# Performance work log

Hardware: AMD Instinct MI355X
Metric: run time of the kernel (lower is better)

Reference implementation:

```python
import jax, jax.numpy as jnp
import numpy as np

TOPK = 20
BN_EPS = 1e-5
NEG_SLOPE = 0.2  # DGL GAT default leaky_relu slope


def setup_inputs() -> dict:
    B, N, Ft, D = 128, 512, 64, 64
    key = jax.random.key(0)
    ks = jax.random.split(key, 6)
    return {
        "data": jax.random.normal(ks[0], (B, N, Ft), jnp.float32),
        "emb": jax.random.normal(ks[1], (N, D), jnp.float32) * 0.5,
        "fc_w": jax.random.normal(ks[2], (D, Ft), jnp.float32) * (1.0 / np.sqrt(Ft)),
        "fc_b": jnp.zeros((D,), jnp.float32),
        "attn_w": jax.random.normal(ks[3], (4 * D,), jnp.float32) * (1.0 / np.sqrt(4 * D)),
        "attn_b": jnp.zeros((), jnp.float32),
        "bn_gamma": jnp.ones((D,), jnp.float32),
        "bn_beta": jnp.zeros((D,), jnp.float32),
        "out_w": jax.random.normal(ks[4], (D,), jnp.float32) * (1.0 / np.sqrt(D)),
        "out_b": jnp.zeros((), jnp.float32),
    }


def reference(data, emb, fc_w, fc_b, attn_w, attn_b, bn_gamma, bn_beta, out_w, out_b):
    B, N, Ft = data.shape
    D = emb.shape[-1]

    # --- dynamic graph build from detached embeddings (cosine-sim topk) ---
    w = jax.lax.stop_gradient(emb)
    nrm = jnp.linalg.norm(w, axis=-1)
    cos = (w @ w.T) / (nrm[:, None] * nrm[None, :])      # [N, N]
    _, topk_idx = jax.lax.top_k(cos, TOPK)               # [N, TOPK]
    src = topk_idx.reshape(-1)                           # gated_j (message sources)
    dst = jnp.tile(jnp.arange(N), TOPK)                  # gated_i = arange(N).repeat(1,topk).flatten()

    # --- GAT layer: z = W x + b ; edge score from concat([z, emb]) at both ends ---
    z = jnp.einsum("bnf,df->bnd", data, fc_w) + fc_b     # [B, N, D]
    key_feat = jnp.concatenate([z, jnp.broadcast_to(emb, (B, N, D))], axis=-1)  # [B, N, 2D]
    a_src, a_dst = attn_w[: 2 * D], attn_w[2 * D :]
    s_src = jnp.einsum("bnd,d->bn", key_feat, a_src)
    s_dst = jnp.einsum("bnd,d->bn", key_feat, a_dst)
    e = jax.nn.leaky_relu(s_src[:, src] + s_dst[:, dst] + attn_b, NEG_SLOPE)    # [B, E]

    # segment softmax over incoming edges of each dst node (same edges every batch)
    m = jnp.full((B, N), -jnp.inf, e.dtype).at[:, dst].max(e)
    p = jnp.exp(e - m[:, dst])
    denom = jnp.zeros((B, N), e.dtype).at[:, dst].add(p)
    alpha = p / denom[:, dst]                            # [B, E]

    # scatter-aggregate messages
    h = jnp.zeros_like(z).at[:, dst].add(alpha[..., None] * z[:, src])          # [B, N, D]

    # --- trailing dense: mul by embedding, BatchNorm1d over channel D, relu, linear ---
    rst = h * emb[None]                                  # [B, N, D]
    mu = rst.mean(axis=(0, 1))
    var = rst.var(axis=(0, 1))
    rst = jax.nn.relu((rst - mu) / jnp.sqrt(var + BN_EPS) * bn_gamma + bn_beta)
    out = jnp.einsum("bnd,d->bn", rst, out_w) + out_b    # [B, N]
    return out
```

## Files before the change

### kernel.cpp

```cpp
#include <hip/hip_runtime.h>
#include <hip/hip_bf16.h>

#define NN 512
#define DD 64
#define TOPK 20
#define BB 128

__global__ __launch_bounds__(256) void kdot_pre(const float* __restrict__ emb,
                                                const float* __restrict__ attn_w,
                                                double* __restrict__ cosM,
                                                double* __restrict__ nrm,
                                                float* __restrict__ es_src,
                                                float* __restrict__ es_dst,
                                                double* __restrict__ gstats) {
    __shared__ __align__(16) char smem[17408];
    const int bid = blockIdx.x, t = threadIdx.x;

    if (bid < 256) {
        const int bi0 = (bid >> 4) * 32;
        const int bj0 = (bid & 15) * 32;
        float4* A4 = (float4*)smem;
        float4* B4 = (float4*)(smem + 8704);
        const float4* e4 = (const float4*)emb;

        for (int m = t; m < 512; m += 256) {
            const int r = m >> 4, c = m & 15;
            A4[r * 17 + c] = e4[(bi0 + r) * 16 + c];
            B4[r * 17 + c] = e4[(bj0 + r) * 16 + c];
        }
        __syncthreads();

        const int tr = t >> 4, tc = t & 15;
        #pragma unroll
        for (int rr = 0; rr < 2; ++rr) {
            #pragma unroll
            for (int cc = 0; cc < 2; ++cc) {
                const int r  = tr + rr * 16;
                const int cl = tc + cc * 16;
                double dot = 0.0;
                #pragma unroll
                for (int c = 0; c < 16; ++c) {
                    const float4 a = A4[r * 17 + c];
                    const float4 b = B4[cl * 17 + c];
                    dot += (double)a.x * (double)b.x;
                    dot += (double)a.y * (double)b.y;
                    dot += (double)a.z * (double)b.z;
                    dot += (double)a.w * (double)b.w;
                }
                cosM[(long)(bi0 + r) * NN + (bj0 + cl)] = dot;
            }
        }
    } else if (bid < 258) {
        const int j = (bid - 256) * 256 + t;
        const float4* e4 = (const float4*)emb;
        double s = 0.0;
        #pragma unroll
        for (int c = 0; c < 16; ++c) {
            const float4 v = e4[j * 16 + c];
            const double vx = v.x, vy = v.y, vz = v.z, vw = v.w;
            s += vx * vx; s += vy * vy; s += vz * vz; s += vw * vw;
        }
        nrm[j] = sqrt(s);
        if (bid == 256 && t < 128) gstats[t] = 0.0;
    } else {
        const int j = (bid - 258) * 256 + t;
        float s1 = 0.f, s2 = 0.f;
        #pragma unroll
        for (int c = 0; c < 64; ++c) {
            const float w = emb[j * 64 + c];
            s1 += w * attn_w[64 + c];
            s2 += w * attn_w[192 + c];
        }
        es_src[j] = s1;
        es_dst[j] = s2;
    }
}

__global__ __launch_bounds__(256) void kgemm_sel(const float* __restrict__ data,
                                                 const float* __restrict__ fc_w,
                                                 const float* __restrict__ fc_b,
                                                 const float* __restrict__ attn_w,
                                                 const double* __restrict__ cosM,
                                                 const double* __restrict__ nrmArr,
                                                 float* __restrict__ z,
                                                 float* __restrict__ zsrc,
                                                 float* __restrict__ zdst,
                                                 int* __restrict__ topk) {
    __shared__ __align__(16) char smem[34816];
    const int bid = blockIdx.x, t = threadIdx.x;

    if (bid < 1024) {
        float (*As)[68]  = (float(*)[68])smem;
        float (*WsT)[68] = (float(*)[68])(smem + 17408);
        const long r0 = (long)bid * 64;
        const float4* data4 = (const float4*)data;
        const float4* fcw4  = (const float4*)fc_w;

        for (int m = t; m < 1024; m += 256) {
            const int r = m >> 4, c4 = m & 15;
            *(float4*)&As[r][c4 * 4] = data4[(r0 + r) * 16 + c4];
        }
        for (int m = t; m < 1024; m += 256) {
            const int d = m >> 4, f4 = m & 15;
            float4 v = fcw4[d * 16 + f4];
            WsT[f4 * 4 + 0][d] = v.x;
            WsT[f4 * 4 + 1][d] = v.y;
            WsT[f4 * 4 + 2][d] = v.z;
            WsT[f4 * 4 + 3][d] = v.w;
        }
        __syncthreads();

        const int tr = t >> 4, tc = t & 15;
        float acc[4][4] = {};
        for (int k0 = 0; k0 < 64; k0 += 4) {
            float4 a4[4], b4[4];
            #pragma unroll
            for (int i = 0; i < 4; ++i) a4[i] = *(float4*)&As[tr * 4 + i][k0];
            #pragma unroll
            for (int kk = 0; kk < 4; ++kk) b4[kk] = *(float4*)&WsT[k0 + kk][tc * 4];
            #pragma unroll
            for (int i = 0; i < 4; ++i) {
                acc[i][0] += a4[i].x * b4[0].x + a4[i].y * b4[1].x + a4[i].z * b4[2].x + a4[i].w * b4[3].x;
                acc[i][1] += a4[i].x * b4[0].y + a4[i].y * b4[1].y + a4[i].z * b4[2].y + a4[i].w * b4[3].y;
                acc[i][2] += a4[i].x * b4[0].z + a4[i].y * b4[1].z + a4[i].z * b4[2].z + a4[i].w * b4[3].z;
                acc[i][3] += a4[i].x * b4[0].w + a4[i].y * b4[1].w + a4[i].z * b4[2].w + a4[i].w * b4[3].w;
            }
        }
        float bias[4], aw0[4], aw2[4];
        #pragma unroll
        for (int j = 0; j < 4; ++j) {
            bias[j] = fc_b[tc * 4 + j];
            aw0[j]  = attn_w[tc * 4 + j];
            aw2[j]  = attn_w[128 + tc * 4 + j];
        }
        float zb[4][4];
        #pragma unroll
        for (int i = 0; i < 4; ++i) {
            #pragma unroll
            for (int j = 0; j < 4; ++j) zb[i][j] = acc[i][j] + bias[j];
            float4 vv; vv.x = zb[i][0]; vv.y = zb[i][1]; vv.z = zb[i][2]; vv.w = zb[i][3];
            *(float4*)&z[(r0 + tr * 4 + i) * 64 + tc * 4] = vv;
        }
        __syncthreads();

        float (*redA)[17] = (float(*)[17])smem;
        float (*redB)[17] = (float(*)[17])(smem + 4352);
        #pragma unroll
        for (int i = 0; i < 4; ++i) {
            redA[tr * 4 + i][tc] = zb[i][0] * aw0[0] + zb[i][1] * aw0[1] + zb[i][2] * aw0[2] + zb[i][3] * aw0[3];
            redB[tr * 4 + i][tc] = zb[i][0] * aw2[0] + zb[i][1] * aw2[1] + zb[i][2] * aw2[2] + zb[i][3] * aw2[3];
        }
        __syncthreads();
        if (t < 64) {
            float sA = 0.f, sB = 0.f;
            #pragma unroll
            for (int k = 0; k < 16; ++k) { sA += redA[t][k]; sB += redB[t][k]; }
            zsrc[r0 + t] = sA;
            zdst[r0 + t] = sB;
        }
    } else {
        const int wid = t >> 6, lane = t & 63;
        const int i = (bid - 1024) * 4 + wid;

        const double nrm_i = nrmArr[i];
        double v[8];
        #pragma unroll
        for (int s = 0; s < 8; ++s)
            v[s] = cosM[(long)i * NN + s * 64 + lane] / (nrm_i * nrmArr[s * 64 + lane]);

        for (int k = 0; k < TOPK; ++k) {
            double bv = v[0]; int bs = 0;
            #pragma unroll
            for (int s = 1; s < 8; ++s) if (v[s] > bv) { bv = v[s]; bs = s; }
            int bi = bs * 64 + lane;
            #pragma unroll
            for (int off = 32; off > 0; off >>= 1) {
                double ov = __shfl_xor(bv, off);
                int    oi = __shfl_xor(bi, off);
                if (ov > bv || (ov == bv && oi < bi)) { bv = ov; bi = oi; }
            }
            if (lane == 0) topk[i * TOPK + k] = bi;
            if ((bi & 63) == lane) v[bi >> 6] = -1e300;
        }
    }
}

__global__ __launch_bounds__(256) void k3_attn(const float* __restrict__ z,
                                               const float* __restrict__ zsrc,
                                               const float* __restrict__ zdst,
                                               const float* __restrict__ es_src,
                                               const float* __restrict__ es_dst,
                                               const int* __restrict__ topk,
                                               const float* __restrict__ emb,
                                               const float* __restrict__ attn_b_p,
                                               float* __restrict__ rst,
                                               double* __restrict__ gstats) {
    __shared__ float  zs[512 * 16];
    __shared__ double alf_pool[2560];
    __shared__ unsigned short sIdx[256 * 20];
    float* alf = (float*)alf_pool;
    const float4* alf4 = (const float4*)alf_pool;

    const int b    = blockIdx.x >> 2;
    const int dq   = blockIdx.x & 3;
    const int doff = dq * 16;
    const int t    = threadIdx.x;
    const float attn_b = *attn_b_p;
    const long b512 = (long)b * NN;

    float4* zs4 = (float4*)zs;
    for (int m = t; m < 2048; m += 256) {
        const int n = m >> 2, c4i = m & 3;
        zs4[m] = *(const float4*)(z + (b512 + n) * 64 + doff + c4i * 4);
    }
    __syncthreads();

    const int c4 = t & 3;
    const int rq = t >> 2;
    double s1[4] = {0,0,0,0}, s2[4] = {0,0,0,0};

    for (int chunk = 0; chunk < 2; ++chunk) {
        {
            const int n = chunk * 256 + t;
            const float sd = zdst[b512 + n] + es_dst[n] + attn_b;
            float ev[TOPK];
            float m0 = -1e30f;
            #pragma unroll
            for (int tt = 0; tt < TOPK; ++tt) {
                const int s = topk[n + tt * NN];
                sIdx[t * TOPK + tt] = (unsigned short)s;
                float e = zsrc[b512 + s] + es_src[s] + sd;
                e = (e >= 0.f) ? e : 0.2f * e;
                ev[tt] = e;
                m0 = fmaxf(m0, e);
            }
            float dsum = 0.f;
            #pragma unroll
            for (int tt = 0; tt < TOPK; ++tt) { ev[tt] = __expf(ev[tt] - m0); dsum += ev[tt]; }
            const float inv = 1.0f / dsum;
            #pragma unroll
            for (int tt = 0; tt < TOPK; ++tt) alf[t * TOPK + tt] = ev[tt] * inv;
        }
        __syncthreads();

        #pragma unroll
        for (int it = 0; it < 4; ++it) {
            const int nl = it * 64 + rq;
            const int n  = chunk * 256 + nl;
            float4 af[5];
            #pragma unroll
            for (int q = 0; q < 5; ++q) af[q] = alf4[nl * 5 + q];
            const float* av = (const float*)af;
            float4 acc = {0.f, 0.f, 0.f, 0.f};
            #pragma unroll
            for (int tt = 0; tt < TOPK; ++tt) {
                const float a = av[tt];
                const float4 zv = zs4[(int)sIdx[nl * TOPK + tt] * 4 + c4];
                acc.x += a * zv.x; acc.y += a * zv.y; acc.z += a * zv.z; acc.w += a * zv.w;
            }
            const float4 ev = *(const float4*)&emb[n * 64 + doff + c4 * 4];
            float4 r;
            r.x = acc.x * ev.x; r.y = acc.y * ev.y; r.z = acc.z * ev.z; r.w = acc.w * ev.w;
            *(float4*)&rst[(b512 + n) * 64 + doff + c4 * 4] = r;
            s1[0] += (double)r.x; s2[0] += (double)r.x * (double)r.x;
            s1[1] += (double)r.y; s2[1] += (double)r.y * (double)r.y;
            s1[2] += (double)r.z; s2[2] += (double)r.z * (double)r.z;
            s1[3] += (double)r.w; s2[3] += (double)r.w * (double)r.w;
        }
        __syncthreads();
    }

    double* r1 = alf_pool;
    double* r2 = alf_pool + 1024;
    #pragma unroll
    for (int j = 0; j < 4; ++j) {
        r1[(c4 * 4 + j) * 64 + rq] = s1[j];
        r2[(c4 * 4 + j) * 64 + rq] = s2[j];
    }
    __syncthreads();
    if (t < 16) {
        double a = 0.0, bb = 0.0;
        for (int q = 0; q < 64; ++q) { a += r1[t * 64 + q]; bb += r2[t * 64 + q]; }
        atomicAdd(&gstats[doff + t], a);
        atomicAdd(&gstats[64 + doff + t], bb);
    }
}

__global__ __launch_bounds__(256) void k5_out(const float* __restrict__ rst,
                                              const double* __restrict__ gstats,
                                              const float* __restrict__ gamma,
                                              const float* __restrict__ beta,
                                              const float* __restrict__ out_w,
                                              const float* __restrict__ out_b_p,
                                              float* __restrict__ out) {
    __shared__ float scv[64], biv[64];
    const int t = threadIdx.x;
    if (t < 64) {
        const double M = (double)BB * (double)NN;
        const double s  = gstats[t];
        const double s2 = gstats[64 + t];
        const double mu  = s / M;
        const double var = s2 / M - mu * mu;
        const float scale = (float)((double)gamma[t] / sqrt(var + 1e-5));
        scv[t] = scale;
        biv[t] = beta[t] - (float)mu * scale;
    }
    __syncthreads();

    const int wid = t >> 6, lane = t & 63;
    const float sc = scv[lane], bi = biv[lane], ow = out_w[lane];
    const float ob = *out_b_p;
    const long rowbase = (long)blockIdx.x * 16 + wid * 4;
    float v[4];
    #pragma unroll
    for (int rr = 0; rr < 4; ++rr)
        v[rr] = fmaxf(rst[(rowbase + rr) * 64 + lane] * sc + bi, 0.f) * ow;
    #pragma unroll
    for (int off = 32; off > 0; off >>= 1)
        #pragma unroll
        for (int rr = 0; rr < 4; ++rr) v[rr] += __shfl_down(v[rr], off);
    if (lane == 0)
        #pragma unroll
        for (int rr = 0; rr < 4; ++rr) out[rowbase + rr] = v[rr] + ob;
}

extern "C" void kernel_launch(void* const* d_in, const int* in_sizes, int n_in,
                              void* d_out, int out_size, void* d_ws, size_t ws_size,
                              hipStream_t stream) {
    const float* data   = (const float*)d_in[0];
    const float* emb    = (const float*)d_in[1];
    const float* fc_w   = (const float*)d_in[2];
    const float* fc_b   = (const float*)d_in[3];
    const float* attn_w = (const float*)d_in[4];
    const float* attn_b = (const float*)d_in[5];
    const float* gamma  = (const float*)d_in[6];
    const float* beta   = (const float*)d_in[7];
    const float* out_w  = (const float*)d_in[8];
    const float* out_b  = (const float*)d_in[9];
    float* out = (float*)d_out;

    char* ws = (char*)d_ws;
    float*  z      = (float*) (ws + 0);
    float*  rst    = (float*) (ws + 16777216);
    float*  zsrc   = (float*) (ws + 33554432);
    float*  zdst   = (float*) (ws + 33816576);
    int*    topk   = (int*)   (ws + 34078720);
    float*  es_src = (float*) (ws + 34119680);
    float*  es_dst = (float*) (ws + 34121728);
    double* gstats = (double*)(ws + 34123776);
    double* nrm    = (double*)(ws + 34124800);
    double* cosM   = (double*)(ws + 34131968);

    kdot_pre<<<260, 256, 0, stream>>>(emb, attn_w, cosM, nrm, es_src, es_dst, gstats);
    kgemm_sel<<<1152, 256, 0, stream>>>(data, fc_w, fc_b, attn_w, cosM, nrm,
                                        z, zsrc, zdst, topk);
    k3_attn<<<BB * 4, 256, 0, stream>>>(z, zsrc, zdst, es_src, es_dst, topk, emb,
                                        attn_b, rst, gstats);
    k5_out<<<4096, 256, 0, stream>>>(rst, gstats, gamma, beta, out_w, out_b, out);
}
```

Baseline: 142.1 us.

## Fuse cosine-sim, norm and top-k selection into the GEMM kernel launch

Merges the separate dot-product/norm precompute kernel into the GEMM+selection kernel, so one launch fewer runs. Each top-k block now computes its own cosine row and all 512 norms in shared memory instead of reading a global double cosM matrix. This removes a kernel boundary and the global round trip of the 512x512 double matrix. In exchange each of the 512 selection blocks redundantly recomputes all row norms, and per-row work uses only one wave for the selection.

Result: no change. 140.3 us (-1.3%).

```diff
diff --git a/kernel.cpp b/kernel.cpp
--- a/kernel.cpp
+++ b/kernel.cpp
@@ -1,91 +1,22 @@
 #include <hip/hip_runtime.h>
-#include <hip/hip_bf16.h>
 
 #define NN 512
 #define DD 64
 #define TOPK 20
 #define BB 128
 
-__global__ __launch_bounds__(256) void kdot_pre(const float* __restrict__ emb,
-                                                const float* __restrict__ attn_w,
-                                                double* __restrict__ cosM,
-                                                double* __restrict__ nrm,
-                                                float* __restrict__ es_src,
-                                                float* __restrict__ es_dst,
-                                                double* __restrict__ gstats) {
-    __shared__ __align__(16) char smem[17408];
-    const int bid = blockIdx.x, t = threadIdx.x;
-
-    if (bid < 256) {
-        const int bi0 = (bid >> 4) * 32;
-        const int bj0 = (bid & 15) * 32;
-        float4* A4 = (float4*)smem;
-        float4* B4 = (float4*)(smem + 8704);
-        const float4* e4 = (const float4*)emb;
-
-        for (int m = t; m < 512; m += 256) {
-            const int r = m >> 4, c = m & 15;
-            A4[r * 17 + c] = e4[(bi0 + r) * 16 + c];
-            B4[r * 17 + c] = e4[(bj0 + r) * 16 + c];
-        }
-        __syncthreads();
-
-        const int tr = t >> 4, tc = t & 15;
-        #pragma unroll
-        for (int rr = 0; rr < 2; ++rr) {
-            #pragma unroll
-            for (int cc = 0; cc < 2; ++cc) {
-                const int r  = tr + rr * 16;
-                const int cl = tc + cc * 16;
-                double dot = 0.0;
-                #pragma unroll
-                for (int c = 0; c < 16; ++c) {
-                    const float4 a = A4[r * 17 + c];
-                    const float4 b = B4[cl * 17 + c];
-                    dot += (double)a.x * (double)b.x;
-                    dot += (double)a.y * (double)b.y;
-                    dot += (double)a.z * (double)b.z;
-                    dot += (double)a.w * (double)b.w;
-                }
-                cosM[(long)(bi0 + r) * NN + (bj0 + cl)] = dot;
-            }
-        }
-    } else if (bid < 258) {
-        const int j = (bid - 256) * 256 + t;
-        const float4* e4 = (const float4*)emb;
-        double s = 0.0;
-        #pragma unroll
-        for (int c = 0; c < 16; ++c) {
-            const float4 v = e4[j * 16 + c];
-            const double vx = v.x, vy = v.y, vz = v.z, vw = v.w;
-            s += vx * vx; s += vy * vy; s += vz * vz; s += vw * vw;
-        }
-        nrm[j] = sqrt(s);
-        if (bid == 256 && t < 128) gstats[t] = 0.0;
-    } else {
-        const int j = (bid - 258) * 256 + t;
-        float s1 = 0.f, s2 = 0.f;
-        #pragma unroll
-        for (int c = 0; c < 64; ++c) {
-            const float w = emb[j * 64 + c];
-            s1 += w * attn_w[64 + c];
-            s2 += w * attn_w[192 + c];
-        }
-        es_src[j] = s1;
-        es_dst[j] = s2;
-    }
-}
-
-__global__ __launch_bounds__(256) void kgemm_sel(const float* __restrict__ data,
-                                                 const float* __restrict__ fc_w,
-                                                 const float* __restrict__ fc_b,
-                                                 const float* __restrict__ attn_w,
-                                                 const double* __restrict__ cosM,
-                                                 const double* __restrict__ nrmArr,
-                                                 float* __restrict__ z,
-                                                 float* __restrict__ zsrc,
-                                                 float* __restrict__ zdst,
-                                                 int* __restrict__ topk) {
+__global__ __launch_bounds__(256) void k1_pre(const float* __restrict__ data,
+                                              const float* __restrict__ emb,
+                                              const float* __restrict__ fc_w,
+                                              const float* __restrict__ fc_b,
+                                              const float* __restrict__ attn_w,
+                                              float* __restrict__ es_src,
+                                              float* __restrict__ es_dst,
+                                              double* __restrict__ gstats,
+                                              float* __restrict__ z,
+                                              float* __restrict__ zsrc,
+                                              float* __restrict__ zdst,
+                                              int* __restrict__ topk) {
     __shared__ __align__(16) char smem[34816];
     const int bid = blockIdx.x, t = threadIdx.x;
 
@@ -158,30 +89,74 @@
             zsrc[r0 + t] = sA;
             zdst[r0 + t] = sB;
         }
+    } else if (bid < 1536) {
+        const int i = bid - 1024;
+        double* cosrow = (double*)smem;
+        double* nrmv   = (double*)(smem + 4096);
+        float4* A4     = (float4*)(smem + 8192);
+        const float4* e4 = (const float4*)emb;
+
+        if (t < 16) A4[t] = e4[i * 16 + t];
+        __syncthreads();
+
+        #pragma unroll
+        for (int jj = 0; jj < 2; ++jj) {
+            const int j = jj * 256 + t;
+            double dot = 0.0, ss = 0.0;
+            #pragma unroll
+            for (int c = 0; c < 16; ++c) {
+                const float4 a = A4[c];
+                const float4 b = e4[j * 16 + c];
+                dot += (double)a.x * (double)b.x;
+                dot += (double)a.y * (double)b.y;
+                dot += (double)a.z * (double)b.z;
+                dot += (double)a.w * (double)b.w;
+                const double vx = b.x, vy = b.y, vz = b.z, vw = b.w;
+                ss += vx * vx; ss += vy * vy; ss += vz * vz; ss += vw * vw;
+            }
+            cosrow[j] = dot;
+            nrmv[j]   = sqrt(ss);
+        }
+        __syncthreads();
+
+        if (t < 64) {
+            const int lane = t;
+            const double nrm_i = nrmv[i];
+            double v[8];
+            #pragma unroll
+            for (int s = 0; s < 8; ++s)
+                v[s] = cosrow[s * 64 + lane] / (nrm_i * nrmv[s * 64 + lane]);
+
+            for (int k = 0; k < TOPK; ++k) {
+                double bv = v[0]; int bs = 0;
+                #pragma unroll
+                for (int s = 1; s < 8; ++s) if (v[s] > bv) { bv = v[s]; bs = s; }
+                int bi2 = bs * 64 + lane;
+                #pragma unroll
+                for (int off = 32; off > 0; off >>= 1) {
+                    double ov = __shfl_xor(bv, off);
+                    int    oi = __shfl_xor(bi2, off);
+                    if (ov > bv || (ov == bv && oi < bi2)) { bv = ov; bi2 = oi; }
+                }
+                if (lane == 0) topk[i * TOPK + k] = bi2;
+                if ((bi2 & 63) == lane) v[bi2 >> 6] = -1e300;
+            }
+        }
     } else {
-        const int wid = t >> 6, lane = t & 63;
-        const int i = (bid - 1024) * 4 + wid;
-
-        const double nrm_i = nrmArr[i];
-        double v[8];
-        #pragma unroll
-        for (int s = 0; s < 8; ++s)
-            v[s] = cosM[(long)i * NN + s * 64 + lane] / (nrm_i * nrmArr[s * 64 + lane]);
-
-        for (int k = 0; k < TOPK; ++k) {
-            double bv = v[0]; int bs = 0;
-            #pragma unroll
-            for (int s = 1; s < 8; ++s) if (v[s] > bv) { bv = v[s]; bs = s; }
-            int bi = bs * 64 + lane;
-            #pragma unroll
-            for (int off = 32; off > 0; off >>= 1) {
-                double ov = __shfl_xor(bv, off);
-                int    oi = __shfl_xor(bi, off);
-                if (ov > bv || (ov == bv && oi < bi)) { bv = ov; bi = oi; }
-            }
-            if (lane == 0) topk[i * TOPK + k] = bi;
-            if ((bi & 63) == lane) v[bi >> 6] = -1e300;
-        }
+        #pragma unroll
+        for (int jj = 0; jj < 2; ++jj) {
+            const int j = jj * 256 + t;
+            float s1 = 0.f, s2 = 0.f;
+            #pragma unroll
+            for (int c = 0; c < 64; ++c) {
+                const float w = emb[j * 64 + c];
+                s1 += w * attn_w[64 + c];
+                s2 += w * attn_w[192 + c];
+            }
+            es_src[j] = s1;
+            es_dst[j] = s2;
+        }
+        if (t < 128) gstats[t] = 0.0;
     }
 }
 
@@ -348,12 +323,10 @@
     float*  es_src = (float*) (ws + 34119680);
     float*  es_dst = (float*) (ws + 34121728);
     double* gstats = (double*)(ws + 34123776);
-    double* nrm    = (double*)(ws + 34124800);
-    double* cosM   = (double*)(ws + 34131968);
-
-    kdot_pre<<<260, 256, 0, stream>>>(emb, attn_w, cosM, nrm, es_src, es_dst, gstats);
-    kgemm_sel<<<1152, 256, 0, stream>>>(data, fc_w, fc_b, attn_w, cosM, nrm,
-                                        z, zsrc, zdst, topk);
+
+    k1_pre<<<1537, 256, 0, stream>>>(data, emb, fc_w, fc_b, attn_w,
+                                     es_src, es_dst, gstats,
+                                     z, zsrc, zdst, topk);
     k3_attn<<<BB * 4, 256, 0, stream>>>(z, zsrc, zdst, es_src, es_dst, topk, emb,
                                         attn_b, rst, gstats);
     k5_out<<<4096, 256, 0, stream>>>(rst, gstats, gamma, beta, out_w, out_b, out);
```
